# Performance work log

Hardware: AMD Instinct MI355X
Metric: run time of the kernel (lower is better)

The kernel has to match this reference:

```python
import jax, jax.numpy as jnp
import numpy as np

# --- fake-quant helpers with straight-through estimator (STE) ---

def _ste(x, xq):
    # identity grad through the rounding
    return x + jax.lax.stop_gradient(xq - x)

def act_quant(x, bit=2):
    # symmetric per-tensor uniform fake-quant of activations
    n = float(2 ** (bit - 1) - 1)  # 2-bit -> 1 level each side
    s = jnp.max(jnp.abs(x)) + 1e-8
    xq = jnp.round(jnp.clip(x / s, -1.0, 1.0) * n) / n * s
    return _ste(x, xq)

def weight_quant(w, bit=2):
    # DoReFa-style low-bit weight fake-quant
    levels = float(2 ** bit - 1)
    wt = jnp.tanh(w)
    wt = wt / (jnp.max(jnp.abs(wt)) + 1e-8)        # in [-1, 1]
    wq = 2.0 * (jnp.round((wt + 1.0) * 0.5 * levels) / levels) - 1.0
    return _ste(wt, wq)

def conv3x3(x, w, b):
    # NCHW, OIHW, stride 1, padding 1
    y = jax.lax.conv_general_dilated(
        x, w, window_strides=(1, 1), padding=((1, 1), (1, 1)),
        dimension_numbers=("NCHW", "OIHW", "NCHW"))
    return y + b[None, :, None, None]


def setup_inputs() -> dict:
    key = jax.random.key(0)
    k1, k2, k3, k4, k5 = jax.random.split(key, 5)
    B, C, H, W = 16, 64, 128, 128
    fan_in = C * 3 * 3
    std = 1.0 / np.sqrt(fan_in)
    return {
        "x": jax.random.normal(k1, (B, C, H, W), dtype=jnp.float32),
        "w1": jax.random.normal(k2, (C, C, 3, 3), dtype=jnp.float32) * std,
        "b1": jax.random.normal(k3, (C,), dtype=jnp.float32) * std,
        "w2": jax.random.normal(k4, (C, C, 3, 3), dtype=jnp.float32) * std,
        "b2": jax.random.normal(k5, (C,), dtype=jnp.float32) * std,
    }


def reference(x, w1, b1, w2, b2):
    A_BIT, W_BIT, RES_SCALE = 2, 2, 1.0
    out = act_quant(x, A_BIT)                 # quant1
    out = conv3x3(out, weight_quant(w1, W_BIT), b1)  # conv1 (low-bit)
    out1 = jax.nn.relu(out)                   # act
    out1 = act_quant(out1, A_BIT)             # quant2
    res = conv3x3(out1, weight_quant(w2, W_BIT), b2) # conv2 (low-bit)
    return res * RES_SCALE + x                # scaled residual add
```

## Files before the change

### kernel.cpp

```cpp
#include <hip/hip_runtime.h>
#include <math.h>

#define NB 16
#define CC 64
#define HH 128
#define WW 128
#define NPIX (NB*CC*HH*WW)
#define WELEM (CC*CC*9)

#define TRR 8
#define TCC 16
#define HRR 10
#define HCC 18
#define HPX (HRR*HCC)
#define PL  (HH*WW)

#define PYY 132
#define PXX 130
#define XQIMG (PYY*PXX*64)
#define XQTOT (NB*XQIMG)

#define S2OFF 512

typedef __attribute__((ext_vector_type(4))) int   int32x4;
typedef __attribute__((ext_vector_type(8))) short short8_t;

__device__ __forceinline__ int lds_a(int pix, int q) {
    return pix * 64 + ((q ^ ((pix >> 1) & 3)) << 4);
}

__device__ __forceinline__ float read_s1(const unsigned* scal) {
    float m = 0.f;
    #pragma unroll
    for (int i = 0; i < 32; ++i) m = fmaxf(m, __uint_as_float(scal[i * 16]));
    return m + 1e-8f;
}

__device__ __forceinline__ float max4(float4 v) {
    return fmaxf(fmaxf(fabsf(v.x), fabsf(v.y)), fmaxf(fabsf(v.z), fabsf(v.w)));
}

__global__ __launch_bounds__(256) void k_reduce(const float* __restrict__ x,
                                                const float* __restrict__ w1,
                                                const float* __restrict__ w2,
                                                unsigned* __restrict__ scal,
                                                signed char* __restrict__ o1,
                                                signed char* __restrict__ o2) {
    __shared__ float red[4];
    const int tid = threadIdx.x;
    if (blockIdx.x < 2048) {
        const float4* x4 = (const float4*)x;
        const int base = blockIdx.x * 2048 + tid;
        float4 v0 = x4[base];
        float4 v1 = x4[base + 256];
        float4 v2 = x4[base + 512];
        float4 v3 = x4[base + 768];
        float4 v4 = x4[base + 1024];
        float4 v5 = x4[base + 1280];
        float4 v6 = x4[base + 1536];
        float4 v7 = x4[base + 1792];
        float a0 = fmaxf(max4(v0), max4(v1));
        float a1 = fmaxf(max4(v2), max4(v3));
        float a2 = fmaxf(max4(v4), max4(v5));
        float a3 = fmaxf(max4(v6), max4(v7));
        float m = fmaxf(fmaxf(a0, a1), fmaxf(a2, a3));
        #pragma unroll
        for (int o = 32; o; o >>= 1) m = fmaxf(m, __shfl_down(m, o, 64));
        if ((tid & 63) == 0) red[tid >> 6] = m;
        __syncthreads();
        if (tid == 0) {
            float v = fmaxf(fmaxf(red[0], red[1]), fmaxf(red[2], red[3]));
            atomicMax(&scal[(blockIdx.x & 31) * 16], __float_as_uint(v));
        }
    } else {
        const int wb = blockIdx.x - 2048;
        const int ten = wb >> 4;
        const int sl  = wb & 15;
        const float* __restrict__ w = ten ? w2 : w1;
        signed char* __restrict__ w8 = ten ? o2 : o1;

        const float4* w4 = (const float4*)w;
        float m = 0.f;
        #pragma unroll
        for (int k = 0; k < 9; ++k) {
            float4 a = w4[tid + (k * 4 + 0) * 256];
            float4 b = w4[tid + (k * 4 + 1) * 256];
            float4 c = w4[tid + (k * 4 + 2) * 256];
            float4 d = w4[tid + (k * 4 + 3) * 256];
            m = fmaxf(m, fmaxf(fmaxf(max4(a), max4(b)), fmaxf(max4(c), max4(d))));
        }
        #pragma unroll
        for (int o = 32; o; o >>= 1) m = fmaxf(m, __shfl_down(m, o, 64));
        if ((tid & 63) == 0) red[tid >> 6] = m;
        __syncthreads();
        float mx = fmaxf(fmaxf(red[0], red[1]), fmaxf(red[2], red[3]));
        float inv = 1.f / (tanhf(mx) + 1e-8f);

        #pragma unroll
        for (int j = 0; j < 9; ++j) {
            int i = sl * 2304 + j * 256 + tid;
            float wt = tanhf(w[i]) * inv;
            float r  = rintf((wt + 1.f) * 1.5f);
            int oc = i / 576, rem = i % 576, ic = rem / 9, tap = rem % 9;
            int lane2 = (oc & 15) | ((ic >> 4) << 4);
            w8[(((oc >> 4) * 9 + tap) * 64 + lane2) * 16 + (ic & 15)] =
                (signed char)(int)(2.f * r - 3.f);
        }
    }
}

__global__ __launch_bounds__(256) void k_quantx(const float* __restrict__ x,
                                                const unsigned* __restrict__ scal,
                                                signed char* __restrict__ xq) {
    __shared__ signed char ldsA[64 * 68];
    __shared__ int ldsB[64 * 16];
    const int tid = threadIdx.x;
    const int n = blockIdx.z, y = blockIdx.y, s = blockIdx.x;
    const float inv_s1 = 1.f / read_s1(scal);

    {
        const int ic = tid >> 2, g = tid & 3;
        const float* __restrict__ src =
            x + (((size_t)n * CC + ic) * HH + y) * WW + s * 64 + g * 16;
        unsigned dw[4];
        #pragma unroll
        for (int q = 0; q < 4; ++q) {
            float4 v = *(const float4*)(src + q * 4);
            float e[4] = {v.x, v.y, v.z, v.w};
            unsigned d = 0;
            #pragma unroll
            for (int j = 0; j < 4; ++j) {
                int qq = (int)rintf(fminf(fmaxf(e[j] * inv_s1, -1.f), 1.f));
                d |= (unsigned)(qq & 255) << (8 * j);
            }
            dw[q] = d;
        }
        *(int4*)(ldsA + ic * 68 + g * 16) = *(const int4*)dw;
    }
    __syncthreads();
    #pragma unroll
    for (int i = 0; i < 4; ++i) {
        int idx = tid + i * 256;
        int d = idx & 15, p = idx >> 4;
        const signed char* a = ldsA + (d * 4) * 68 + p;
        unsigned b0 = (unsigned char)a[0];
        unsigned b1 = (unsigned char)a[68];
        unsigned b2 = (unsigned char)a[136];
        unsigned b3 = (unsigned char)a[204];
        ldsB[p * 16 + d] = (int)(b0 | (b1 << 8) | (b2 << 16) | (b3 << 24));
    }
    __syncthreads();
    signed char* dst = xq + ((size_t)n * PYY + (y + 1)) * (PXX * 64)
                          + (size_t)(1 + s * 64) * 64;
    ((int4*)dst)[tid] = ((const int4*)ldsB)[tid];
}

__global__ __launch_bounds__(256, 5) void k_conv1(
    const signed char* __restrict__ xq,
    const signed char* __restrict__ w8,
    const float* __restrict__ bias,
    unsigned* __restrict__ scal,
    short* __restrict__ accout)
{
    __shared__ float redm[4];
    const int tid = threadIdx.x;
    const int n   = blockIdx.z;
    const int oy0 = blockIdx.y * TRR;
    const int ox0 = blockIdx.x * TCC;
    const float s1 = read_s1(scal);

    const int w     = tid >> 6;
    const int lane  = tid & 63;
    const int lq    = lane >> 4;
    const int lc    = lane & 15;
    const int rbase = w * 2;

    const signed char* __restrict__ A0 = xq + (size_t)n * XQIMG
        + ((size_t)(oy0 + rbase) * PXX + ox0 + lc) * 64 + lq * 16;
    const signed char* __restrict__ W0 = w8 + (size_t)lane * 16;

    int32x4 acc[2][4] = {};
    #pragma unroll 3
    for (int tap = 0; tap < 9; ++tap) {
        const int ky = tap / 3, kx = tap % 3;
        int32x4 b0 = *(const int32x4*)(W0 + (size_t)(0 * 9 + tap) * 1024);
        int32x4 b1 = *(const int32x4*)(W0 + (size_t)(1 * 9 + tap) * 1024);
        int32x4 b2 = *(const int32x4*)(W0 + (size_t)(2 * 9 + tap) * 1024);
        int32x4 b3 = *(const int32x4*)(W0 + (size_t)(3 * 9 + tap) * 1024);
        const signed char* ar = A0 + (ky * PXX + kx) * 64;
        #pragma unroll
        for (int j = 0; j < 2; ++j) {
            int32x4 a = *(const int32x4*)(ar + j * (PXX * 64));
            acc[j][0] = __builtin_amdgcn_mfma_i32_16x16x64_i8(a, b0, acc[j][0], 0, 0, 0);
            acc[j][1] = __builtin_amdgcn_mfma_i32_16x16x64_i8(a, b1, acc[j][1], 0, 0, 0);
            acc[j][2] = __builtin_amdgcn_mfma_i32_16x16x64_i8(a, b2, acc[j][2], 0, 0, 0);
            acc[j][3] = __builtin_amdgcn_mfma_i32_16x16x64_i8(a, b3, acc[j][3], 0, 0, 0);
        }
    }

    const float sc = s1 * (1.f / 3.f);
    float m2 = 0.f;
    #pragma unroll
    for (int j = 0; j < 2; ++j) {
        const int yy = oy0 + rbase + j;
        const size_t pbase = (((size_t)n * HH + yy) * WW + (ox0 + lq * 4)) * 64;
        #pragma unroll
        for (int g = 0; g < 4; ++g) {
            const float bo = bias[g * 16 + lc];
            #pragma unroll
            for (int e = 0; e < 4; ++e) {
                int v = acc[j][g][e];
                m2 = fmaxf(m2, sc * (float)v + bo);
                accout[pbase + (size_t)e * 64 + g * 16 + lc] = (short)v;
            }
        }
    }
    #pragma unroll
    for (int o = 32; o; o >>= 1) m2 = fmaxf(m2, __shfl_down(m2, o, 64));
    if (lane == 0) redm[w] = m2;
    __syncthreads();
    if (tid == 0) {
        float v = fmaxf(fmaxf(redm[0], redm[1]), fmaxf(redm[2], redm[3]));
        int slot = (blockIdx.x + blockIdx.y * 8 + blockIdx.z) & 7;
        atomicMax(&scal[S2OFF + slot * 32], __float_as_uint(v));
    }
}

__global__ __launch_bounds__(256, 5) void k_conv2(
    const float* __restrict__ x,
    const short* __restrict__ accin,
    const signed char* __restrict__ w8,
    const float* __restrict__ bias,
    const float* __restrict__ b1v,
    const unsigned* __restrict__ scal,
    float* __restrict__ out)
{
    __shared__ signed char sA[HPX * 64] __attribute__((aligned(16)));

    const int tid = threadIdx.x;
    const int n   = blockIdx.z;
    const int oy0 = blockIdx.y * TRR;
    const int ox0 = blockIdx.x * TCC;

    const float s1 = read_s1(scal);
    float mx = 0.f;
    #pragma unroll
    for (int i = 0; i < 8; ++i) mx = fmaxf(mx, __uint_as_float(scal[S2OFF + i * 32]));
    const float s2v = mx + 1e-8f;
    const float half_s2 = 0.5f * s2v;
    const float sc1 = s1 * (1.f / 3.f);

    if (tid < HPX) {
        const int r = tid / HCC, c = tid - r * HCC;
        const int y  = oy0 - 1 + r;
        const int xx = ox0 - 1 + c;
        unsigned pk[16];
        #pragma unroll
        for (int d = 0; d < 16; ++d) pk[d] = 0;
        if (y >= 0 && y < HH && xx >= 0 && xx < WW) {
            const short8_t* __restrict__ ap =
                (const short8_t*)(accin + (((size_t)n * HH + y) * WW + xx) * 64);
            #pragma unroll
            for (int k = 0; k < 8; ++k) {
                short8_t sv = ap[k];
                float4 bA = *(const float4*)(b1v + k * 8);
                float4 bB = *(const float4*)(b1v + k * 8 + 4);
                float ba[8] = {bA.x, bA.y, bA.z, bA.w, bB.x, bB.y, bB.z, bB.w};
                #pragma unroll
                for (int e = 0; e < 8; ++e) {
                    float fv = sc1 * (float)sv[e] + ba[e];
                    if (fv >= half_s2) pk[2 * k + (e >> 2)] |= 1u << ((e & 3) * 8);
                }
            }
        }
        #pragma unroll
        for (int q = 0; q < 4; ++q) {
            int4 wv;
            wv.x = (int)pk[4 * q];     wv.y = (int)pk[4 * q + 1];
            wv.z = (int)pk[4 * q + 2]; wv.w = (int)pk[4 * q + 3];
            *(int4*)(sA + lds_a(tid, q)) = wv;
        }
    }
    __syncthreads();

    const int w     = tid >> 6;
    const int lane  = tid & 63;
    const int lq    = lane >> 4;
    const int lc    = lane & 15;
    const int rbase = w * 2;
    const signed char* __restrict__ W0 = w8 + (size_t)lane * 16;

    int32x4 acc[2][4] = {};
    __builtin_amdgcn_s_setprio(1);
    #pragma unroll 3
    for (int tap = 0; tap < 9; ++tap) {
        const int ky = tap / 3, kx = tap % 3;
        int32x4 b0 = *(const int32x4*)(W0 + (size_t)(0 * 9 + tap) * 1024);
        int32x4 b1 = *(const int32x4*)(W0 + (size_t)(1 * 9 + tap) * 1024);
        int32x4 b2 = *(const int32x4*)(W0 + (size_t)(2 * 9 + tap) * 1024);
        int32x4 b3 = *(const int32x4*)(W0 + (size_t)(3 * 9 + tap) * 1024);
        #pragma unroll
        for (int j = 0; j < 2; ++j) {
            int pix = (rbase + j + ky) * HCC + kx + lc;
            int32x4 a = *(const int32x4*)(sA + lds_a(pix, lq));
            acc[j][0] = __builtin_amdgcn_mfma_i32_16x16x64_i8(a, b0, acc[j][0], 0, 0, 0);
            acc[j][1] = __builtin_amdgcn_mfma_i32_16x16x64_i8(a, b1, acc[j][1], 0, 0, 0);
            acc[j][2] = __builtin_amdgcn_mfma_i32_16x16x64_i8(a, b2, acc[j][2], 0, 0, 0);
            acc[j][3] = __builtin_amdgcn_mfma_i32_16x16x64_i8(a, b3, acc[j][3], 0, 0, 0);
        }
    }
    __builtin_amdgcn_s_setprio(0);

    const float sc = s2v * (1.f / 3.f);
    const size_t imgbase = (size_t)n * CC * PL;

    #pragma unroll
    for (int j = 0; j < 2; ++j) {
        const int yy = oy0 + rbase + j;
        const int xb = ox0 + lq * 4;
        #pragma unroll
        for (int g = 0; g < 4; ++g) {
            const int oc = g * 16 + lc;
            const float bo = bias[oc];
            size_t p = imgbase + (size_t)oc * PL + yy * WW + xb;
            float4 xa = *(const float4*)(x + p);
            float4 r;
            r.x = sc * (float)acc[j][g][0] + bo + xa.x;
            r.y = sc * (float)acc[j][g][1] + bo + xa.y;
            r.z = sc * (float)acc[j][g][2] + bo + xa.z;
            r.w = sc * (float)acc[j][g][3] + bo + xa.w;
            *(float4*)(out + p) = r;
        }
    }
}

extern "C" void kernel_launch(void* const* d_in, const int* in_sizes, int n_in,
                              void* d_out, int out_size, void* d_ws, size_t ws_size,
                              hipStream_t stream) {
    const float* x  = (const float*)d_in[0];
    const float* w1 = (const float*)d_in[1];
    const float* b1 = (const float*)d_in[2];
    const float* w2 = (const float*)d_in[3];
    const float* b2 = (const float*)d_in[4];
    float* out = (float*)d_out;

    unsigned*    scal  = (unsigned*)d_ws;
    signed char* w8_1  = (signed char*)d_ws + 4096;
    signed char* w8_2  = w8_1 + WELEM;
    short*       acc16 = (short*)((char*)d_ws + 131072);
    signed char* xq    = (signed char*)d_out;

    hipMemsetAsync(d_ws, 0, 4096, stream);
    hipMemsetAsync(d_out, 0, XQTOT, stream);

    k_reduce<<<2080, 256, 0, stream>>>(x, w1, w2, scal, w8_1, w8_2);
    k_quantx<<<dim3(2, HH, NB), 256, 0, stream>>>(x, scal, xq);

    dim3 grid(WW / TCC, HH / TRR, NB);
    k_conv1<<<grid, 256, 0, stream>>>(xq, w8_1, b1, scal, acc16);
    k_conv2<<<grid, 256, 0, stream>>>(x, acc16, w8_2, b2, b1, scal, out);
}
```

Before: 114.8 us.

## Zero only xq padding border, swizzle conv grids, double-buffer conv2 tiles

Drops the full-buffer memset of the padded quantized activation and instead has 16 extra k_reduce blocks zero only the halo rows and columns, which k_quantx never writes. conv1 and conv2 move to 1D grids with XCD-style block swizzling. Each conv2 block now processes two vertically adjacent 8-row tiles with two LDS buffers, so loading and binarizing the second tile's halo overlaps the MFMA work on the first. Occupancy drops to 4 blocks per CU and LDS use per block doubles.

```diff
diff --git a/kernel.cpp b/kernel.cpp
--- a/kernel.cpp
+++ b/kernel.cpp
@@ -18,7 +18,6 @@
 #define PYY 132
 #define PXX 130
 #define XQIMG (PYY*PXX*64)
-#define XQTOT (NB*XQIMG)
 
 #define S2OFF 512
 
@@ -45,7 +44,8 @@
                                                 const float* __restrict__ w2,
                                                 unsigned* __restrict__ scal,
                                                 signed char* __restrict__ o1,
-                                                signed char* __restrict__ o2) {
+                                                signed char* __restrict__ o2,
+                                                signed char* __restrict__ xq) {
     __shared__ float red[4];
     const int tid = threadIdx.x;
     if (blockIdx.x < 2048) {
@@ -72,7 +72,7 @@
             float v = fmaxf(fmaxf(red[0], red[1]), fmaxf(red[2], red[3]));
             atomicMax(&scal[(blockIdx.x & 31) * 16], __float_as_uint(v));
         }
-    } else {
+    } else if (blockIdx.x < 2080) {
         const int wb = blockIdx.x - 2048;
         const int ten = wb >> 4;
         const int sl  = wb & 15;
@@ -105,6 +105,24 @@
             int lane2 = (oc & 15) | ((ic >> 4) << 4);
             w8[(((oc >> 4) * 9 + tap) * 64 + lane2) * 16 + (ic & 15)] =
                 (signed char)(int)(2.f * r - 3.f);
+        }
+    } else {
+        const int n = blockIdx.x - 2080;
+        for (int t = tid; t < 776; t += 256) {
+            int r, c;
+            if (t < 520) {
+                int r4 = t / 130;
+                r = (r4 == 0) ? 0 : 128 + r4;
+                c = t - r4 * 130;
+            } else {
+                int u = t - 520;
+                r = 1 + (u >> 1);
+                c = (u & 1) ? 129 : 0;
+            }
+            int4* dst = (int4*)(xq + ((size_t)n * PYY + r) * (PXX * 64)
+                                   + (size_t)c * 64);
+            int4 z = {0, 0, 0, 0};
+            dst[0] = z; dst[1] = z; dst[2] = z; dst[3] = z;
         }
     }
 }
@@ -164,9 +182,13 @@
 {
     __shared__ float redm[4];
     const int tid = threadIdx.x;
-    const int n   = blockIdx.z;
-    const int oy0 = blockIdx.y * TRR;
-    const int ox0 = blockIdx.x * TCC;
+    const int bid = blockIdx.x;
+    const int swz = (bid & 7) * 256 + (bid >> 3);
+    const int tx  = swz & 7;
+    const int ty  = (swz >> 3) & 15;
+    const int n   = swz >> 7;
+    const int oy0 = ty * TRR;
+    const int ox0 = tx * TCC;
     const float s1 = read_s1(scal);
 
     const int w     = tid >> 6;
@@ -221,77 +243,55 @@
     __syncthreads();
     if (tid == 0) {
         float v = fmaxf(fmaxf(redm[0], redm[1]), fmaxf(redm[2], redm[3]));
-        int slot = (blockIdx.x + blockIdx.y * 8 + blockIdx.z) & 7;
-        atomicMax(&scal[S2OFF + slot * 32], __float_as_uint(v));
-    }
-}
-
-__global__ __launch_bounds__(256, 5) void k_conv2(
-    const float* __restrict__ x,
-    const short* __restrict__ accin,
-    const signed char* __restrict__ w8,
-    const float* __restrict__ bias,
-    const float* __restrict__ b1v,
-    const unsigned* __restrict__ scal,
-    float* __restrict__ out)
-{
-    __shared__ signed char sA[HPX * 64] __attribute__((aligned(16)));
-
-    const int tid = threadIdx.x;
-    const int n   = blockIdx.z;
-    const int oy0 = blockIdx.y * TRR;
-    const int ox0 = blockIdx.x * TCC;
-
-    const float s1 = read_s1(scal);
-    float mx = 0.f;
-    #pragma unroll
-    for (int i = 0; i < 8; ++i) mx = fmaxf(mx, __uint_as_float(scal[S2OFF + i * 32]));
-    const float s2v = mx + 1e-8f;
-    const float half_s2 = 0.5f * s2v;
-    const float sc1 = s1 * (1.f / 3.f);
-
-    if (tid < HPX) {
-        const int r = tid / HCC, c = tid - r * HCC;
-        const int y  = oy0 - 1 + r;
-        const int xx = ox0 - 1 + c;
-        unsigned pk[16];
-        #pragma unroll
-        for (int d = 0; d < 16; ++d) pk[d] = 0;
-        if (y >= 0 && y < HH && xx >= 0 && xx < WW) {
-            const short8_t* __restrict__ ap =
-                (const short8_t*)(accin + (((size_t)n * HH + y) * WW + xx) * 64);
+        atomicMax(&scal[S2OFF + (swz & 7) * 32], __float_as_uint(v));
+    }
+}
+
+__device__ __forceinline__ bool stage_load(const short* __restrict__ accin,
+    int n, int oy0, int ox0, int sr, int scx, bool sact, short8_t ld[8]) {
+    int y  = oy0 - 1 + sr;
+    int xx = ox0 - 1 + scx;
+    bool v = sact & (y >= 0) & (y < HH) & (xx >= 0) & (xx < WW);
+    int yc = v ? y : 0, xc = v ? xx : 0;
+    const short8_t* __restrict__ ap =
+        (const short8_t*)(accin + (((size_t)n * HH + yc) * WW + xc) * 64);
+    #pragma unroll
+    for (int k = 0; k < 8; ++k) ld[k] = ap[k];
+    return v;
+}
+
+__device__ __forceinline__ void binarize_store(signed char* sbuf, int tid,
+    const short8_t ld[8], bool v, const float* __restrict__ b1v,
+    float sc1, float half_s2) {
+    unsigned pk[16];
+    #pragma unroll
+    for (int d = 0; d < 16; ++d) pk[d] = 0;
+    if (v) {
+        #pragma unroll
+        for (int k = 0; k < 8; ++k) {
+            short8_t sv = ld[k];
+            float4 bA = *(const float4*)(b1v + k * 8);
+            float4 bB = *(const float4*)(b1v + k * 8 + 4);
+            float ba[8] = {bA.x, bA.y, bA.z, bA.w, bB.x, bB.y, bB.z, bB.w};
             #pragma unroll
-            for (int k = 0; k < 8; ++k) {
-                short8_t sv = ap[k];
-                float4 bA = *(const float4*)(b1v + k * 8);
-                float4 bB = *(const float4*)(b1v + k * 8 + 4);
-                float ba[8] = {bA.x, bA.y, bA.z, bA.w, bB.x, bB.y, bB.z, bB.w};
-                #pragma unroll
-                for (int e = 0; e < 8; ++e) {
-                    float fv = sc1 * (float)sv[e] + ba[e];
-                    if (fv >= half_s2) pk[2 * k + (e >> 2)] |= 1u << ((e & 3) * 8);
-                }
+            for (int e = 0; e < 8; ++e) {
+                float fv = sc1 * (float)sv[e] + ba[e];
+                if (fv >= half_s2) pk[2 * k + (e >> 2)] |= 1u << ((e & 3) * 8);
             }
         }
-        #pragma unroll
-        for (int q = 0; q < 4; ++q) {
-            int4 wv;
-            wv.x = (int)pk[4 * q];     wv.y = (int)pk[4 * q + 1];
-            wv.z = (int)pk[4 * q + 2]; wv.w = (int)pk[4 * q + 3];
-            *(int4*)(sA + lds_a(tid, q)) = wv;
-        }
-    }
-    __syncthreads();
-
-    const int w     = tid >> 6;
-    const int lane  = tid & 63;
-    const int lq    = lane >> 4;
-    const int lc    = lane & 15;
-    const int rbase = w * 2;
-    const signed char* __restrict__ W0 = w8 + (size_t)lane * 16;
-
-    int32x4 acc[2][4] = {};
-    __builtin_amdgcn_s_setprio(1);
+    }
+    #pragma unroll
+    for (int q = 0; q < 4; ++q) {
+        int4 wv;
+        wv.x = (int)pk[4 * q];     wv.y = (int)pk[4 * q + 1];
+        wv.z = (int)pk[4 * q + 2]; wv.w = (int)pk[4 * q + 3];
+        *(int4*)(sbuf + lds_a(tid, q)) = wv;
+    }
+}
+
+__device__ __forceinline__ void conv2_mfma(const signed char* __restrict__ sbuf,
+    const signed char* __restrict__ W0, int rbase, int lq, int lc,
+    int32x4 acc[2][4]) {
     #pragma unroll 3
     for (int tap = 0; tap < 9; ++tap) {
         const int ky = tap / 3, kx = tap % 3;
@@ -302,18 +302,20 @@
         #pragma unroll
         for (int j = 0; j < 2; ++j) {
             int pix = (rbase + j + ky) * HCC + kx + lc;
-            int32x4 a = *(const int32x4*)(sA + lds_a(pix, lq));
+            int32x4 a = *(const int32x4*)(sbuf + lds_a(pix, lq));
             acc[j][0] = __builtin_amdgcn_mfma_i32_16x16x64_i8(a, b0, acc[j][0], 0, 0, 0);
             acc[j][1] = __builtin_amdgcn_mfma_i32_16x16x64_i8(a, b1, acc[j][1], 0, 0, 0);
             acc[j][2] = __builtin_amdgcn_mfma_i32_16x16x64_i8(a, b2, acc[j][2], 0, 0, 0);
             acc[j][3] = __builtin_amdgcn_mfma_i32_16x16x64_i8(a, b3, acc[j][3], 0, 0, 0);
         }
     }
-    __builtin_amdgcn_s_setprio(0);
-
-    const float sc = s2v * (1.f / 3.f);
+}
+
+__device__ __forceinline__ void conv2_epi(float* __restrict__ out,
+    const float* __restrict__ x, const float* __restrict__ bias, float sc,
+    int n, int oy0, int ox0, int rbase, int lq, int lc,
+    const int32x4 acc[2][4]) {
     const size_t imgbase = (size_t)n * CC * PL;
-
     #pragma unroll
     for (int j = 0; j < 2; ++j) {
         const int yy = oy0 + rbase + j;
@@ -334,6 +336,68 @@
     }
 }
 
+__global__ __launch_bounds__(256, 4) void k_conv2(
+    const float* __restrict__ x,
+    const short* __restrict__ accin,
+    const signed char* __restrict__ w8,
+    const float* __restrict__ bias,
+    const float* __restrict__ b1v,
+    const unsigned* __restrict__ scal,
+    float* __restrict__ out)
+{
+    __shared__ signed char sA0[HPX * 64] __attribute__((aligned(16)));
+    __shared__ signed char sA1[HPX * 64] __attribute__((aligned(16)));
+
+    const int tid = threadIdx.x;
+    const int bid = blockIdx.x;
+    const int swz = (bid & 7) * 128 + (bid >> 3);
+    const int tx  = swz & 7;
+    const int typ = (swz >> 3) & 7;
+    const int n   = swz >> 6;
+    const int ox0 = tx * TCC;
+    const int oyA = typ * 16;
+    const int oyB = oyA + 8;
+
+    const float s1 = read_s1(scal);
+    float mx = 0.f;
+    #pragma unroll
+    for (int i = 0; i < 8; ++i) mx = fmaxf(mx, __uint_as_float(scal[S2OFF + i * 32]));
+    const float s2v = mx + 1e-8f;
+    const float half_s2 = 0.5f * s2v;
+    const float sc1 = s1 * (1.f / 3.f);
+    const float sc  = s2v * (1.f / 3.f);
+
+    const int w     = tid >> 6;
+    const int lane  = tid & 63;
+    const int lq    = lane >> 4;
+    const int lc    = lane & 15;
+    const int rbase = w * 2;
+    const int sr  = tid / HCC;
+    const int scx = tid - sr * HCC;
+    const bool sact = tid < HPX;
+    const signed char* __restrict__ W0 = w8 + (size_t)lane * 16;
+
+    short8_t ld[8];
+    bool v0 = stage_load(accin, n, oyA, ox0, sr, scx, sact, ld);
+    if (sact) binarize_store(sA0, tid, ld, v0, b1v, sc1, half_s2);
+    __syncthreads();
+
+    bool v1 = stage_load(accin, n, oyB, ox0, sr, scx, sact, ld);
+
+    {
+        int32x4 acc[2][4] = {};
+        conv2_mfma(sA0, W0, rbase, lq, lc, acc);
+        if (sact) binarize_store(sA1, tid, ld, v1, b1v, sc1, half_s2);
+        conv2_epi(out, x, bias, sc, n, oyA, ox0, rbase, lq, lc, acc);
+    }
+    __syncthreads();
+    {
+        int32x4 acc[2][4] = {};
+        conv2_mfma(sA1, W0, rbase, lq, lc, acc);
+        conv2_epi(out, x, bias, sc, n, oyB, ox0, rbase, lq, lc, acc);
+    }
+}
+
 extern "C" void kernel_launch(void* const* d_in, const int* in_sizes, int n_in,
                               void* d_out, int out_size, void* d_ws, size_t ws_size,
                               hipStream_t stream) {
@@ -351,12 +415,9 @@
     signed char* xq    = (signed char*)d_out;
 
     hipMemsetAsync(d_ws, 0, 4096, stream);
-    hipMemsetAsync(d_out, 0, XQTOT, stream);
-
-    k_reduce<<<2080, 256, 0, stream>>>(x, w1, w2, scal, w8_1, w8_2);
+
+    k_reduce<<<2096, 256, 0, stream>>>(x, w1, w2, scal, w8_1, w8_2, xq);
     k_quantx<<<dim3(2, HH, NB), 256, 0, stream>>>(x, scal, xq);
-
-    dim3 grid(WW / TCC, HH / TRR, NB);
-    k_conv1<<<grid, 256, 0, stream>>>(xq, w8_1, b1, scal, acc16);
-    k_conv2<<<grid, 256, 0, stream>>>(x, acc16, w8_2, b2, b1, scal, out);
-}
+    k_conv1<<<2048, 256, 0, stream>>>(xq, w8_1, b1, scal, acc16);
+    k_conv2<<<1024, 256, 0, stream>>>(x, acc16, w8_2, b2, b1, scal, out);
+}
```

Measured after the change: 97.71 us (median of 2 runs). 14.9% less time.

## Split binarization into its own pass, zero only halo borders, swizzle block order

Applied to the files above, without the earlier changes.

The second activation quantization moves out of conv2's LDS prologue into a separate k_binarize kernel. It writes a padded int8 image into workspace, so conv2 reads its A operand straight from global memory the same way conv1 does, and each halo pixel is no longer recomputed by neighbouring tiles. The full memset of the padded xq buffer is replaced by extra k_reduce blocks that zero only the border pixels of both padded buffers. Both conv kernels switch to a 1D grid with a swizzled block order aimed at L2 locality. The cost is one more kernel launch and an extra round trip of the int8 intermediate through global memory.

```diff
diff --git a/kernel.cpp b/kernel.cpp
--- a/kernel.cpp
+++ b/kernel.cpp
@@ -10,9 +10,6 @@
 
 #define TRR 8
 #define TCC 16
-#define HRR 10
-#define HCC 18
-#define HPX (HRR*HCC)
 #define PL  (HH*WW)
 
 #define PYY 132
@@ -24,10 +21,6 @@
 
 typedef __attribute__((ext_vector_type(4))) int   int32x4;
 typedef __attribute__((ext_vector_type(8))) short short8_t;
-
-__device__ __forceinline__ int lds_a(int pix, int q) {
-    return pix * 64 + ((q ^ ((pix >> 1) & 3)) << 4);
-}
 
 __device__ __forceinline__ float read_s1(const unsigned* scal) {
     float m = 0.f;
@@ -45,7 +38,9 @@
                                                 const float* __restrict__ w2,
                                                 unsigned* __restrict__ scal,
                                                 signed char* __restrict__ o1,
-                                                signed char* __restrict__ o2) {
+                                                signed char* __restrict__ o2,
+                                                signed char* __restrict__ xq,
+                                                signed char* __restrict__ xb) {
     __shared__ float red[4];
     const int tid = threadIdx.x;
     if (blockIdx.x < 2048) {
@@ -72,7 +67,7 @@
             float v = fmaxf(fmaxf(red[0], red[1]), fmaxf(red[2], red[3]));
             atomicMax(&scal[(blockIdx.x & 31) * 16], __float_as_uint(v));
         }
-    } else {
+    } else if (blockIdx.x < 2080) {
         const int wb = blockIdx.x - 2048;
         const int ten = wb >> 4;
         const int sl  = wb & 15;
@@ -105,6 +100,26 @@
             int lane2 = (oc & 15) | ((ic >> 4) << 4);
             w8[(((oc >> 4) * 9 + tap) * 64 + lane2) * 16 + (ic & 15)] =
                 (signed char)(int)(2.f * r - 3.f);
+        }
+    } else {
+        const bool isB = blockIdx.x >= 2096;
+        const int n = blockIdx.x - (isB ? 2096 : 2080);
+        signed char* __restrict__ base = isB ? xb : xq;
+        for (int t = tid; t < 776; t += 256) {
+            int r, c;
+            if (t < 520) {
+                int r4 = t / 130;
+                r = (r4 == 0) ? 0 : 128 + r4;
+                c = t - r4 * 130;
+            } else {
+                int u = t - 520;
+                r = 1 + (u >> 1);
+                c = (u & 1) ? 129 : 0;
+            }
+            int4* dst = (int4*)(base + ((size_t)n * PYY + r) * (PXX * 64)
+                                     + (size_t)c * 64);
+            int4 z = {0, 0, 0, 0};
+            dst[0] = z; dst[1] = z; dst[2] = z; dst[3] = z;
         }
     }
 }
@@ -164,9 +179,13 @@
 {
     __shared__ float redm[4];
     const int tid = threadIdx.x;
-    const int n   = blockIdx.z;
-    const int oy0 = blockIdx.y * TRR;
-    const int ox0 = blockIdx.x * TCC;
+    const int bid = blockIdx.x;
+    const int swz = (bid & 7) * 256 + (bid >> 3);
+    const int tx  = swz & 7;
+    const int ty  = (swz >> 3) & 15;
+    const int n   = swz >> 7;
+    const int oy0 = ty * TRR;
+    const int ox0 = tx * TCC;
     const float s1 = read_s1(scal);
 
     const int w     = tid >> 6;
@@ -221,77 +240,89 @@
     __syncthreads();
     if (tid == 0) {
         float v = fmaxf(fmaxf(redm[0], redm[1]), fmaxf(redm[2], redm[3]));
-        int slot = (blockIdx.x + blockIdx.y * 8 + blockIdx.z) & 7;
-        atomicMax(&scal[S2OFF + slot * 32], __float_as_uint(v));
+        atomicMax(&scal[S2OFF + (swz & 7) * 32], __float_as_uint(v));
+    }
+}
+
+__global__ __launch_bounds__(256) void k_binarize(
+    const short* __restrict__ accin,
+    const float* __restrict__ b1v,
+    const unsigned* __restrict__ scal,
+    signed char* __restrict__ xb)
+{
+    const int gp = blockIdx.x * 256 + threadIdx.x;
+    const int n  = gp >> 14;
+    const int rm = gp & 16383;
+    const int y  = rm >> 7;
+    const int xx = rm & 127;
+
+    const float s1 = read_s1(scal);
+    float mx = 0.f;
+    #pragma unroll
+    for (int i = 0; i < 8; ++i) mx = fmaxf(mx, __uint_as_float(scal[S2OFF + i * 32]));
+    const float half_s2 = 0.5f * (mx + 1e-8f);
+    const float sc1 = s1 * (1.f / 3.f);
+
+    const short8_t* __restrict__ ap = (const short8_t*)(accin + (size_t)gp * 64);
+    unsigned pk[16];
+    #pragma unroll
+    for (int d = 0; d < 16; ++d) pk[d] = 0;
+    #pragma unroll
+    for (int k = 0; k < 8; ++k) {
+        short8_t sv = ap[k];
+        float4 bA = *(const float4*)(b1v + k * 8);
+        float4 bB = *(const float4*)(b1v + k * 8 + 4);
+        float ba[8] = {bA.x, bA.y, bA.z, bA.w, bB.x, bB.y, bB.z, bB.w};
+        #pragma unroll
+        for (int e = 0; e < 8; ++e) {
+            float fv = sc1 * (float)sv[e] + ba[e];
+            if (fv >= half_s2) pk[2 * k + (e >> 2)] |= 1u << ((e & 3) * 8);
+        }
+    }
+    signed char* dst = xb + ((size_t)n * PYY + (y + 1)) * (PXX * 64)
+                          + (size_t)(xx + 1) * 64;
+    #pragma unroll
+    for (int q = 0; q < 4; ++q) {
+        int4 wv;
+        wv.x = (int)pk[4 * q];     wv.y = (int)pk[4 * q + 1];
+        wv.z = (int)pk[4 * q + 2]; wv.w = (int)pk[4 * q + 3];
+        *(int4*)(dst + q * 16) = wv;
     }
 }
 
 __global__ __launch_bounds__(256, 5) void k_conv2(
     const float* __restrict__ x,
-    const short* __restrict__ accin,
+    const signed char* __restrict__ xb,
     const signed char* __restrict__ w8,
     const float* __restrict__ bias,
-    const float* __restrict__ b1v,
     const unsigned* __restrict__ scal,
     float* __restrict__ out)
 {
-    __shared__ signed char sA[HPX * 64] __attribute__((aligned(16)));
-
     const int tid = threadIdx.x;
-    const int n   = blockIdx.z;
-    const int oy0 = blockIdx.y * TRR;
-    const int ox0 = blockIdx.x * TCC;
-
-    const float s1 = read_s1(scal);
+    const int bid = blockIdx.x;
+    const int swz = (bid & 7) * 256 + (bid >> 3);
+    const int tx  = swz & 7;
+    const int ty  = (swz >> 3) & 15;
+    const int n   = swz >> 7;
+    const int oy0 = ty * TRR;
+    const int ox0 = tx * TCC;
+
     float mx = 0.f;
     #pragma unroll
     for (int i = 0; i < 8; ++i) mx = fmaxf(mx, __uint_as_float(scal[S2OFF + i * 32]));
-    const float s2v = mx + 1e-8f;
-    const float half_s2 = 0.5f * s2v;
-    const float sc1 = s1 * (1.f / 3.f);
-
-    if (tid < HPX) {
-        const int r = tid / HCC, c = tid - r * HCC;
-        const int y  = oy0 - 1 + r;
-        const int xx = ox0 - 1 + c;
-        unsigned pk[16];
-        #pragma unroll
-        for (int d = 0; d < 16; ++d) pk[d] = 0;
-        if (y >= 0 && y < HH && xx >= 0 && xx < WW) {
-            const short8_t* __restrict__ ap =
-                (const short8_t*)(accin + (((size_t)n * HH + y) * WW + xx) * 64);
-            #pragma unroll
-            for (int k = 0; k < 8; ++k) {
-                short8_t sv = ap[k];
-                float4 bA = *(const float4*)(b1v + k * 8);
-                float4 bB = *(const float4*)(b1v + k * 8 + 4);
-                float ba[8] = {bA.x, bA.y, bA.z, bA.w, bB.x, bB.y, bB.z, bB.w};
-                #pragma unroll
-                for (int e = 0; e < 8; ++e) {
-                    float fv = sc1 * (float)sv[e] + ba[e];
-                    if (fv >= half_s2) pk[2 * k + (e >> 2)] |= 1u << ((e & 3) * 8);
-                }
-            }
-        }
-        #pragma unroll
-        for (int q = 0; q < 4; ++q) {
-            int4 wv;
-            wv.x = (int)pk[4 * q];     wv.y = (int)pk[4 * q + 1];
-            wv.z = (int)pk[4 * q + 2]; wv.w = (int)pk[4 * q + 3];
-            *(int4*)(sA + lds_a(tid, q)) = wv;
-        }
-    }
-    __syncthreads();
+    const float sc = (mx + 1e-8f) * (1.f / 3.f);
 
     const int w     = tid >> 6;
     const int lane  = tid & 63;
     const int lq    = lane >> 4;
     const int lc    = lane & 15;
     const int rbase = w * 2;
+
+    const signed char* __restrict__ A0 = xb + (size_t)n * XQIMG
+        + ((size_t)(oy0 + rbase) * PXX + ox0 + lc) * 64 + lq * 16;
     const signed char* __restrict__ W0 = w8 + (size_t)lane * 16;
 
     int32x4 acc[2][4] = {};
-    __builtin_amdgcn_s_setprio(1);
     #pragma unroll 3
     for (int tap = 0; tap < 9; ++tap) {
         const int ky = tap / 3, kx = tap % 3;
@@ -299,30 +330,27 @@
         int32x4 b1 = *(const int32x4*)(W0 + (size_t)(1 * 9 + tap) * 1024);
         int32x4 b2 = *(const int32x4*)(W0 + (size_t)(2 * 9 + tap) * 1024);
         int32x4 b3 = *(const int32x4*)(W0 + (size_t)(3 * 9 + tap) * 1024);
+        const signed char* ar = A0 + (ky * PXX + kx) * 64;
         #pragma unroll
         for (int j = 0; j < 2; ++j) {
-            int pix = (rbase + j + ky) * HCC + kx + lc;
-            int32x4 a = *(const int32x4*)(sA + lds_a(pix, lq));
+            int32x4 a = *(const int32x4*)(ar + j * (PXX * 64));
             acc[j][0] = __builtin_amdgcn_mfma_i32_16x16x64_i8(a, b0, acc[j][0], 0, 0, 0);
             acc[j][1] = __builtin_amdgcn_mfma_i32_16x16x64_i8(a, b1, acc[j][1], 0, 0, 0);
             acc[j][2] = __builtin_amdgcn_mfma_i32_16x16x64_i8(a, b2, acc[j][2], 0, 0, 0);
             acc[j][3] = __builtin_amdgcn_mfma_i32_16x16x64_i8(a, b3, acc[j][3], 0, 0, 0);
         }
     }
-    __builtin_amdgcn_s_setprio(0);
-
-    const float sc = s2v * (1.f / 3.f);
+
     const size_t imgbase = (size_t)n * CC * PL;
-
     #pragma unroll
     for (int j = 0; j < 2; ++j) {
         const int yy = oy0 + rbase + j;
-        const int xb = ox0 + lq * 4;
+        const int xbs = ox0 + lq * 4;
         #pragma unroll
         for (int g = 0; g < 4; ++g) {
             const int oc = g * 16 + lc;
             const float bo = bias[oc];
-            size_t p = imgbase + (size_t)oc * PL + yy * WW + xb;
+            size_t p = imgbase + (size_t)oc * PL + yy * WW + xbs;
             float4 xa = *(const float4*)(x + p);
             float4 r;
             r.x = sc * (float)acc[j][g][0] + bo + xa.x;
@@ -348,15 +376,14 @@
     signed char* w8_1  = (signed char*)d_ws + 4096;
     signed char* w8_2  = w8_1 + WELEM;
     short*       acc16 = (short*)((char*)d_ws + 131072);
+    signed char* xbuf  = (signed char*)d_ws + 131072 + 33554432;
     signed char* xq    = (signed char*)d_out;
 
     hipMemsetAsync(d_ws, 0, 4096, stream);
-    hipMemsetAsync(d_out, 0, XQTOT, stream);
-
-    k_reduce<<<2080, 256, 0, stream>>>(x, w1, w2, scal, w8_1, w8_2);
+
+    k_reduce<<<2112, 256, 0, stream>>>(x, w1, w2, scal, w8_1, w8_2, xq, xbuf);
     k_quantx<<<dim3(2, HH, NB), 256, 0, stream>>>(x, scal, xq);
-
-    dim3 grid(WW / TCC, HH / TRR, NB);
-    k_conv1<<<grid, 256, 0, stream>>>(xq, w8_1, b1, scal, acc16);
-    k_conv2<<<grid, 256, 0, stream>>>(x, acc16, w8_2, b2, b1, scal, out);
-}
+    k_conv1<<<2048, 256, 0, stream>>>(xq, w8_1, b1, scal, acc16);
+    k_binarize<<<1024, 256, 0, stream>>>(acc16, b1, scal, xbuf);
+    k_conv2<<<2048, 256, 0, stream>>>(x, xbuf, w8_2, b2, scal, out);
+}
```

Result: faster. 111.2 us (-3.2%).
